# Kernel optimization log

Hardware: AMD Instinct MI355X
Metric: run time of the kernel (lower is better)

Reference implementation:

```python
import jax, jax.numpy as jnp
import numpy as np

KTAPS = 10  # kernel_size in StructuredStateSpace.compute_cauchy_kernel


def setup_inputs() -> dict:
    key = jax.random.key(0)
    ks = jax.random.split(key, 6)
    T, B, F, L, OUT = 8192, 16, 32, 16, 128
    return {
        "x": jax.random.normal(ks[0], (T, B, F), dtype=jnp.float32),
        # K[l, s] = C_l @ A_l^s @ B_l, each an (F, F) matrix (in_features == hidden_size)
        "K": jax.random.normal(ks[1], (L, KTAPS, F, F), dtype=jnp.float32),
        # emission_layer[l]: nn.Linear(hidden_size, 1) -> weight (F,), bias scalar per l
        "em_w": jax.random.normal(ks[2], (L, F), dtype=jnp.float32),
        "em_b": jax.random.normal(ks[3], (L,), dtype=jnp.float32),
        # linear_decoder: nn.Linear(L, out_features)
        "dec_w": jax.random.normal(ks[4], (OUT, L), dtype=jnp.float32),
        "dec_b": jax.random.normal(ks[5], (OUT,), dtype=jnp.float32),
    }


def reference(x, K, em_w, em_b, dec_w, dec_b):
    # x: (T, B, F); K: (L, KTAPS, F, F)
    T, B, F = x.shape
    # causal conv: y[l, t] = sum_{s=0}^{min(t, KTAPS-1)} K[l, s] @ x[t - s]
    xp = jnp.pad(x, ((KTAPS - 1, 0), (0, 0), (0, 0)))  # (T+9, B, F)
    # X[s, t] = x[t - s]  -> (KTAPS, T, B, F); loop is over the fixed 10 taps only
    X = jnp.stack([xp[KTAPS - 1 - s:KTAPS - 1 - s + T] for s in range(KTAPS)], axis=0)
    y = jnp.einsum('lsof,stbf->ltbo', K, X)  # (L, T, B, F)
    # per-branch emission Linear(F, 1), stacked over L -> (T, B, L)
    h = jnp.einsum('ltbo,lo->tbl', y, em_w) + em_b
    h = jnp.swapaxes(h, 0, 1)  # (B, T, L)
    # linear_decoder: (B, T, L) -> (B, T, out_features)
    return h @ dec_w.T + dec_b
```

## Files before the change

kernel.cpp:

```cpp
#include <hip/hip_runtime.h>
#include <hip/hip_bf16.h>

typedef __attribute__((ext_vector_type(4))) float f32x4;
typedef __attribute__((ext_vector_type(8))) short bf16x8;
typedef __attribute__((ext_vector_type(4))) short bf16x4;

#define T_DIM 8192
#define B_DIM 16
#define F_DIM 32
#define L_DIM 16
#define NTAPS 10
#define O_DIM 128
#define M_TOTAL (T_DIM * B_DIM)

#define G_OFF    0
#define W2F_OFF  20480
#define BIAS_OFF 102400

static __device__ __forceinline__ unsigned short f2bf(float f) {
    union { float f; unsigned int u; } v; v.f = f;
    unsigned int r = v.u + 0x7fffu + ((v.u >> 16) & 1u);
    return (unsigned short)(r >> 16);
}

__global__ __launch_bounds__(256) void g_stage_kernel(
    const float* __restrict__ K, const float* __restrict__ em_w,
    float* __restrict__ G)
{
    int s = blockIdx.x >> 4, l = blockIdx.x & 15;
    int f = threadIdx.x & 31, opg = threadIdx.x >> 5;
    const float* Kb = K + (size_t)(l * NTAPS + s) * 1024;
    float p = 0.f;
    #pragma unroll
    for (int k = 0; k < 4; ++k) {
        int op = opg * 4 + k;
        p += em_w[l * 32 + op] * Kb[op * 32 + f];
    }
    __shared__ float red[8][32];
    red[opg][f] = p;
    __syncthreads();
    if (threadIdx.x < 32) {
        float g = 0.f;
        #pragma unroll
        for (int q = 0; q < 8; ++q) g += red[q][threadIdx.x];
        G[(s * 16 + l) * 32 + threadIdx.x] = g;
    }
}

__global__ __launch_bounds__(256) void build_w2_kernel(
    const float* __restrict__ G, const float* __restrict__ em_b,
    const float* __restrict__ dec_w, const float* __restrict__ dec_b,
    unsigned short* __restrict__ w2f, float* __restrict__ bias2)
{
    int s = blockIdx.x >> 3, nt = blockIdx.x & 7;
    int lane = threadIdx.x & 63, w = threadIdx.x >> 6;
    int lo = lane & 15, fb = (lane >> 4) * 8;
    int o = nt * 16 + lo;

    float acc[8] = {0.f,0.f,0.f,0.f,0.f,0.f,0.f,0.f};
    #pragma unroll
    for (int l = 0; l < 4; ++l) {
        int ll = w * 4 + l;
        float dw = dec_w[o * L_DIM + ll];
        const float* g = G + (s * 16 + ll) * 32 + fb;
        #pragma unroll
        for (int j = 0; j < 8; ++j) acc[j] += dw * g[j];
    }
    __shared__ float red[4][64][8];
    #pragma unroll
    for (int j = 0; j < 8; ++j) red[w][lane][j] = acc[j];
    __syncthreads();
    if (w == 0) {
        unsigned short o8[8];
        #pragma unroll
        for (int j = 0; j < 8; ++j)
            o8[j] = f2bf(red[0][lane][j] + red[1][lane][j] +
                         red[2][lane][j] + red[3][lane][j]);
        *(bf16x8*)(w2f + ((size_t)(s * 8 + nt) * 64 + lane) * 8) = *(const bf16x8*)o8;
    }
    if (s == 0 && nt == 0 && threadIdx.x < O_DIM) {
        float b = dec_b[threadIdx.x];
        #pragma unroll
        for (int l = 0; l < 16; ++l) b += dec_w[threadIdx.x * L_DIM + l] * em_b[l];
        bias2[threadIdx.x] = b;
    }
}

#define XROWS 272
#define XSTRIDE 80

__global__ __launch_bounds__(512) void s4_main_kernel(
    const float* __restrict__ x, const unsigned short* __restrict__ w2f,
    const float* __restrict__ bias2, float* __restrict__ out)
{
    __shared__ char xlds[XROWS * XSTRIDE];

    int tid  = threadIdx.x;
    int lane = tid & 63, w = tid >> 6;
    int lo = lane & 15, g = lane >> 4;

    int Rb = blockIdx.x * 256;
    int b  = Rb >> 13;
    int t0 = Rb & (T_DIM - 1);

    #pragma unroll
    for (int rep = 0; rep < 5; ++rep) {
        int c = rep * 512 + tid;
        if (c < XROWS * 8) {
            int i = c >> 3, part = c & 7;
            int t = t0 + i - 16;
            unsigned short r4[4] = {0, 0, 0, 0};
            if (t >= 0) {
                f32x4 v = *(const f32x4*)(x + ((size_t)t * B_DIM + b) * F_DIM + part * 4);
                #pragma unroll
                for (int j = 0; j < 4; ++j) r4[j] = f2bf(v[j]);
            }
            *(bf16x4*)(xlds + i * XSTRIDE + part * 8) = *(const bf16x4*)r4;
        }
    }

    f32x4 bias[8];
    #pragma unroll
    for (int nt = 0; nt < 8; ++nt)
        bias[nt] = *(const f32x4*)(bias2 + nt * 16 + g * 4);

    __syncthreads();

    f32x4 acc[2][8];
    #pragma unroll
    for (int mt = 0; mt < 2; ++mt)
        #pragma unroll
        for (int nt = 0; nt < 8; ++nt)
            acc[mt][nt] = (f32x4){0.f, 0.f, 0.f, 0.f};

    int ib = 16 + w * 32 + lo;
    for (int s = 0; s < NTAPS; ++s) {
        bf16x8 wf[8];
        const bf16x8* wp = (const bf16x8*)w2f + (size_t)s * 8 * 64 + lane;
        #pragma unroll
        for (int nt = 0; nt < 8; ++nt) wf[nt] = wp[nt * 64];
        #pragma unroll
        for (int mt = 0; mt < 2; ++mt) {
            bf16x8 xf = *(const bf16x8*)(xlds + (ib + mt * 16 - s) * XSTRIDE + g * 16);
            #pragma unroll
            for (int nt = 0; nt < 8; ++nt)
                acc[mt][nt] = __builtin_amdgcn_mfma_f32_16x16x32_bf16(
                    wf[nt], xf, acc[mt][nt], 0, 0, 0);
        }
    }

    #pragma unroll
    for (int nt = 0; nt < 8; ++nt) {
        #pragma unroll
        for (int mt = 0; mt < 2; ++mt) {
            size_t r = (size_t)Rb + w * 32 + mt * 16 + lo;
            f32x4 v = acc[mt][nt] + bias[nt];
            *(f32x4*)(out + r * O_DIM + nt * 16 + g * 4) = v;
        }
    }
}

extern "C" void kernel_launch(void* const* d_in, const int* in_sizes, int n_in,
                              void* d_out, int out_size, void* d_ws, size_t ws_size,
                              hipStream_t stream)
{
    const float* x     = (const float*)d_in[0];
    const float* K     = (const float*)d_in[1];
    const float* em_w  = (const float*)d_in[2];
    const float* em_b  = (const float*)d_in[3];
    const float* dec_w = (const float*)d_in[4];
    const float* dec_b = (const float*)d_in[5];
    float* out = (float*)d_out;

    float*          Gbuf  = (float*)((char*)d_ws + G_OFF);
    unsigned short* w2f   = (unsigned short*)((char*)d_ws + W2F_OFF);
    float*          bias2 = (float*)((char*)d_ws + BIAS_OFF);

    hipLaunchKernelGGL(g_stage_kernel, dim3(NTAPS * 16), dim3(256), 0, stream,
                       K, em_w, Gbuf);
    hipLaunchKernelGGL(build_w2_kernel, dim3(NTAPS * 8), dim3(256), 0, stream,
                       Gbuf, em_b, dec_w, dec_b, w2f, bias2);
    hipLaunchKernelGGL(s4_main_kernel, dim3(M_TOTAL / 256), dim3(512), 0, stream,
                       x, w2f, bias2, out);
}
```

Measured before the change: 110.0 us.

## Fuse weight-prep kernels and halve main kernel tile to 128 rows

Merges the G-stage and W2-build kernels into one kernel that computes G in shared memory per block, removing a launch and the global round trip through G. The main kernel now uses 256-thread blocks of 128 rows (twice the blocks, smaller LDS halo tile), and loads the bias lazily in the epilogue to reduce register pressure. Each fused block recomputes all 16 G rows for its tap, adding redundant work, and the smaller tiles raise the relative halo overhead.

```diff
diff --git a/kernel.cpp b/kernel.cpp
--- a/kernel.cpp
+++ b/kernel.cpp
@@ -13,9 +13,8 @@
 #define O_DIM 128
 #define M_TOTAL (T_DIM * B_DIM)
 
-#define G_OFF    0
-#define W2F_OFF  20480
-#define BIAS_OFF 102400
+#define W2F_OFF  0
+#define BIAS_OFF 81920
 
 static __device__ __forceinline__ unsigned short f2bf(float f) {
     union { float f; unsigned int u; } v; v.f = f;
@@ -23,73 +22,59 @@
     return (unsigned short)(r >> 16);
 }
 
-__global__ __launch_bounds__(256) void g_stage_kernel(
+__global__ __launch_bounds__(256) void build_w2_fused(
     const float* __restrict__ K, const float* __restrict__ em_w,
-    float* __restrict__ G)
+    const float* __restrict__ em_b, const float* __restrict__ dec_w,
+    const float* __restrict__ dec_b, unsigned short* __restrict__ w2f,
+    float* __restrict__ bias2)
 {
-    int s = blockIdx.x >> 4, l = blockIdx.x & 15;
-    int f = threadIdx.x & 31, opg = threadIdx.x >> 5;
-    const float* Kb = K + (size_t)(l * NTAPS + s) * 1024;
-    float p = 0.f;
+    int s = blockIdx.x >> 3, nt = blockIdx.x & 7;
+    int tid = threadIdx.x;
+
+    __shared__ float Glds[16 * 32];
     #pragma unroll
-    for (int k = 0; k < 4; ++k) {
-        int op = opg * 4 + k;
-        p += em_w[l * 32 + op] * Kb[op * 32 + f];
-    }
-    __shared__ float red[8][32];
-    red[opg][f] = p;
-    __syncthreads();
-    if (threadIdx.x < 32) {
+    for (int rep = 0; rep < 2; ++rep) {
+        int idx = rep * 256 + tid;
+        int l = idx >> 5, f = idx & 31;
+        const float* Kb = K + (size_t)(l * NTAPS + s) * 1024 + f;
+        const float* em = em_w + l * 32;
         float g = 0.f;
         #pragma unroll
-        for (int q = 0; q < 8; ++q) g += red[q][threadIdx.x];
-        G[(s * 16 + l) * 32 + threadIdx.x] = g;
+        for (int op = 0; op < 32; ++op) g += em[op] * Kb[op * 32];
+        Glds[idx] = g;
+    }
+    __syncthreads();
+
+    if (tid < 64) {
+        int lane = tid;
+        int lo = lane & 15, fb = (lane >> 4) * 8;
+        int o = nt * 16 + lo;
+        float acc[8] = {0.f,0.f,0.f,0.f,0.f,0.f,0.f,0.f};
+        #pragma unroll
+        for (int l = 0; l < 16; ++l) {
+            float dw = dec_w[o * L_DIM + l];
+            const float* g = Glds + l * 32 + fb;
+            #pragma unroll
+            for (int j = 0; j < 8; ++j) acc[j] += dw * g[j];
+        }
+        unsigned short o8[8];
+        #pragma unroll
+        for (int j = 0; j < 8; ++j) o8[j] = f2bf(acc[j]);
+        *(bf16x8*)(w2f + ((size_t)(s * 8 + nt) * 64 + lane) * 8) = *(const bf16x8*)o8;
+    }
+    if (s == 0 && nt == 0 && tid >= 128 && tid < 128 + O_DIM) {
+        int o = tid - 128;
+        float b = dec_b[o];
+        #pragma unroll
+        for (int l = 0; l < 16; ++l) b += dec_w[o * L_DIM + l] * em_b[l];
+        bias2[o] = b;
     }
 }
 
-__global__ __launch_bounds__(256) void build_w2_kernel(
-    const float* __restrict__ G, const float* __restrict__ em_b,
-    const float* __restrict__ dec_w, const float* __restrict__ dec_b,
-    unsigned short* __restrict__ w2f, float* __restrict__ bias2)
-{
-    int s = blockIdx.x >> 3, nt = blockIdx.x & 7;
-    int lane = threadIdx.x & 63, w = threadIdx.x >> 6;
-    int lo = lane & 15, fb = (lane >> 4) * 8;
-    int o = nt * 16 + lo;
-
-    float acc[8] = {0.f,0.f,0.f,0.f,0.f,0.f,0.f,0.f};
-    #pragma unroll
-    for (int l = 0; l < 4; ++l) {
-        int ll = w * 4 + l;
-        float dw = dec_w[o * L_DIM + ll];
-        const float* g = G + (s * 16 + ll) * 32 + fb;
-        #pragma unroll
-        for (int j = 0; j < 8; ++j) acc[j] += dw * g[j];
-    }
-    __shared__ float red[4][64][8];
-    #pragma unroll
-    for (int j = 0; j < 8; ++j) red[w][lane][j] = acc[j];
-    __syncthreads();
-    if (w == 0) {
-        unsigned short o8[8];
-        #pragma unroll
-        for (int j = 0; j < 8; ++j)
-            o8[j] = f2bf(red[0][lane][j] + red[1][lane][j] +
-                         red[2][lane][j] + red[3][lane][j]);
-        *(bf16x8*)(w2f + ((size_t)(s * 8 + nt) * 64 + lane) * 8) = *(const bf16x8*)o8;
-    }
-    if (s == 0 && nt == 0 && threadIdx.x < O_DIM) {
-        float b = dec_b[threadIdx.x];
-        #pragma unroll
-        for (int l = 0; l < 16; ++l) b += dec_w[threadIdx.x * L_DIM + l] * em_b[l];
-        bias2[threadIdx.x] = b;
-    }
-}
-
-#define XROWS 272
+#define XROWS 144
 #define XSTRIDE 80
 
-__global__ __launch_bounds__(512) void s4_main_kernel(
+__global__ __launch_bounds__(256) void s4_main_kernel(
     const float* __restrict__ x, const unsigned short* __restrict__ w2f,
     const float* __restrict__ bias2, float* __restrict__ out)
 {
@@ -99,13 +84,13 @@
     int lane = tid & 63, w = tid >> 6;
     int lo = lane & 15, g = lane >> 4;
 
-    int Rb = blockIdx.x * 256;
+    int Rb = blockIdx.x * 128;
     int b  = Rb >> 13;
     int t0 = Rb & (T_DIM - 1);
 
     #pragma unroll
     for (int rep = 0; rep < 5; ++rep) {
-        int c = rep * 512 + tid;
+        int c = rep * 256 + tid;
         if (c < XROWS * 8) {
             int i = c >> 3, part = c & 7;
             int t = t0 + i - 16;
@@ -118,12 +103,6 @@
             *(bf16x4*)(xlds + i * XSTRIDE + part * 8) = *(const bf16x4*)r4;
         }
     }
-
-    f32x4 bias[8];
-    #pragma unroll
-    for (int nt = 0; nt < 8; ++nt)
-        bias[nt] = *(const f32x4*)(bias2 + nt * 16 + g * 4);
-
     __syncthreads();
 
     f32x4 acc[2][8];
@@ -151,10 +130,11 @@
 
     #pragma unroll
     for (int nt = 0; nt < 8; ++nt) {
+        f32x4 bi = *(const f32x4*)(bias2 + nt * 16 + g * 4);
         #pragma unroll
         for (int mt = 0; mt < 2; ++mt) {
             size_t r = (size_t)Rb + w * 32 + mt * 16 + lo;
-            f32x4 v = acc[mt][nt] + bias[nt];
+            f32x4 v = acc[mt][nt] + bi;
             *(f32x4*)(out + r * O_DIM + nt * 16 + g * 4) = v;
         }
     }
@@ -172,14 +152,11 @@
     const float* dec_b = (const float*)d_in[5];
     float* out = (float*)d_out;
 
-    float*          Gbuf  = (float*)((char*)d_ws + G_OFF);
     unsigned short* w2f   = (unsigned short*)((char*)d_ws + W2F_OFF);
     float*          bias2 = (float*)((char*)d_ws + BIAS_OFF);
 
-    hipLaunchKernelGGL(g_stage_kernel, dim3(NTAPS * 16), dim3(256), 0, stream,
-                       K, em_w, Gbuf);
-    hipLaunchKernelGGL(build_w2_kernel, dim3(NTAPS * 8), dim3(256), 0, stream,
-                       Gbuf, em_b, dec_w, dec_b, w2f, bias2);
-    hipLaunchKernelGGL(s4_main_kernel, dim3(M_TOTAL / 256), dim3(512), 0, stream,
+    hipLaunchKernelGGL(build_w2_fused, dim3(NTAPS * 8), dim3(256), 0, stream,
+                       K, em_w, em_b, dec_w, dec_b, w2f, bias2);
+    hipLaunchKernelGGL(s4_main_kernel, dim3(M_TOTAL / 128), dim3(256), 0, stream,
                        x, w2f, bias2, out);
 }
```

Result: slower. 113.8 us (+3.4%).
